# Kernel tuning notes

Hardware: AMD Instinct MI355X
Metric: run time of the kernel (lower is better)

The kernel has to match this reference:

```python
import jax, jax.numpy as jnp
import numpy as np

B, S, D, H = 4, 2048, 1024, 16
DK = D // H
THETA = 10000.0


def _rope(x, token_positions):
    # x: [b, h, s, d_k]; token_positions: [s] int
    half = x.shape[-1] // 2
    freqs = 1.0 / (THETA ** (2.0 * jnp.arange(half, dtype=jnp.float32) / x.shape[-1]))
    angles = token_positions.astype(jnp.float32)[:, None] * freqs[None, :]  # [s, half]
    cos, sin = jnp.cos(angles), jnp.sin(angles)
    x1 = x[..., 0::2]  # interleaved pairing: (d/2, 2)
    x2 = x[..., 1::2]
    r1 = x1 * cos - x2 * sin
    r2 = x2 * cos + x1 * sin
    return jnp.stack([r1, r2], axis=-1).reshape(x.shape)


def setup_inputs() -> dict:
    key = jax.random.key(0)
    ks = jax.random.split(key, 5)
    std_io = np.sqrt(2.0 / (D + D)).astype(np.float32)
    return {
        "x": jax.random.normal(ks[0], (B, S, D), dtype=jnp.float32),
        "token_positions": jnp.arange(S, dtype=jnp.int32),
        "Wq": jax.random.normal(ks[1], (D, D), dtype=jnp.float32) * std_io,
        "Wk": jax.random.normal(ks[2], (D, D), dtype=jnp.float32) * std_io,
        "Wv": jax.random.normal(ks[3], (D, D), dtype=jnp.float32) * std_io,
        "Wo": jax.random.normal(ks[4], (D, D), dtype=jnp.float32) * std_io,
    }


def reference(x, token_positions, Wq, Wk, Wv, Wo):
    b, s, d = x.shape
    # Linear uses W: [out, in] -> y = x @ W.T
    def proj(W):
        y = jnp.einsum('bsd,od->bso', x, W)
        return y.reshape(b, s, H, DK).transpose(0, 2, 1, 3)  # [b,h,s,dk]
    q, k, v = proj(Wq), proj(Wk), proj(Wv)
    q = _rope(q, token_positions)
    k = _rope(k, token_positions)
    scores = jnp.einsum('bhqd,bhkd->bhqk', q, k) / jnp.sqrt(jnp.float32(DK))
    causal = jnp.tril(jnp.ones((s, s), dtype=bool))
    scores = jnp.where(causal, scores, -jnp.inf)
    attn = jax.nn.softmax(scores, axis=-1)
    out = jnp.einsum('bhqk,bhkd->bhqd', attn, v)
    out = out.transpose(0, 2, 1, 3).reshape(b, s, d)
    return jnp.einsum('bsd,od->bso', out, Wo)
```

## Files before the change

### kernel.cpp

```cpp
#include <hip/hip_runtime.h>
#include <math.h>

#define B_ 4
#define S_ 2048
#define D_ 1024
#define H_ 16
#define DK_ 64
#define SCALE_ 0.125f
#define THETA_ 10000.0f
#define LOG2E_ 1.44269504f

typedef unsigned short ushort_t;
typedef __attribute__((ext_vector_type(8))) short bf16x8;
typedef __attribute__((ext_vector_type(4))) float f32x4;

__device__ __forceinline__ ushort_t f2bf(float f) {
    union { float f; unsigned u; } v; v.f = f;
    unsigned r = (v.u + 0x7FFFu + ((v.u >> 16) & 1u)) >> 16;
    return (ushort_t)r;
}

#define GLOAD_LDS16(gptr, lptr)                                                   \
    __builtin_amdgcn_global_load_lds(                                             \
        (const __attribute__((address_space(1))) unsigned int*)(gptr),            \
        (__attribute__((address_space(3))) unsigned int*)(lptr), 16, 0, 0)

__global__ __launch_bounds__(256) void cast_f32_bf16(const float* __restrict__ in,
                                                     ushort_t* __restrict__ out, int n) {
    int i = (blockIdx.x * 256 + threadIdx.x) * 4;
    if (i >= n) return;
    float4 v = *reinterpret_cast<const float4*>(in + i);
    unsigned lo = (unsigned)f2bf(v.x) | ((unsigned)f2bf(v.y) << 16);
    unsigned hi = (unsigned)f2bf(v.z) | ((unsigned)f2bf(v.w) << 16);
    uint2 u; u.x = lo; u.y = hi;
    *reinterpret_cast<uint2*>(out + i) = u;
}

__global__ __launch_bounds__(256) void build_rope(const int* __restrict__ pos,
                                                  float2* __restrict__ tab) {
    int i = blockIdx.x * 256 + threadIdx.x;
    int s = i >> 5, p = i & 31;
    float freq = powf(THETA_, -2.0f * (float)p / 64.0f);
    float a = (float)pos[s] * freq;
    tab[i] = make_float2(cosf(a), sinf(a));
}

template <int MODE>
__global__ __launch_bounds__(256) void gemm_bf16(const ushort_t* __restrict__ A,
                                                 const ushort_t* __restrict__ W,
                                                 const float2* __restrict__ tab,
                                                 float qscale,
                                                 float* __restrict__ outF,
                                                 ushort_t* __restrict__ outB) {
    __shared__ ushort_t Asl[128 * 32];
    __shared__ ushort_t Bsl[128 * 32];

    const int t = threadIdx.x;
    const int lane = t & 63;
    const int w = t >> 6;
    const int lr = lane & 15;
    const int lg = lane >> 4;

    const int bid = blockIdx.x;
    const int swz = (bid & 7) * 64 + (bid >> 3);
    const int m0 = (swz >> 3) * 128;
    const int n0 = (swz & 7) * 128;

    const int wr = w >> 1;
    const int wc = w & 1;

    f32x4 acc[4][4] = {};

    for (int k0 = 0; k0 < D_; k0 += 32) {
#pragma unroll
        for (int i = 0; i < 2; ++i) {
            const int off = w * 2048 + i * 1024 + lane * 16;
            const int row = off >> 6;
            const int col = (off & 63) >> 1;
            GLOAD_LDS16(A + (size_t)(m0 + row) * D_ + k0 + col, Asl + (w * 1024 + i * 512));
            GLOAD_LDS16(W + (size_t)(n0 + row) * D_ + k0 + col, Bsl + (w * 1024 + i * 512));
        }
        __syncthreads();

        bf16x8 af[4], bfr[4];
#pragma unroll
        for (int x = 0; x < 4; ++x) {
            af[x]  = *reinterpret_cast<const bf16x8*>(&Asl[(wr * 64 + x * 16 + lr) * 32 + lg * 8]);
            bfr[x] = *reinterpret_cast<const bf16x8*>(&Bsl[(wc * 64 + x * 16 + lr) * 32 + lg * 8]);
        }
#pragma unroll
        for (int mi = 0; mi < 4; ++mi)
#pragma unroll
            for (int ni = 0; ni < 4; ++ni)
                acc[mi][ni] = __builtin_amdgcn_mfma_f32_16x16x32_bf16(af[mi], bfr[ni], acc[mi][ni], 0, 0, 0);
        __syncthreads();
    }

#pragma unroll
    for (int mi = 0; mi < 4; ++mi) {
#pragma unroll
        for (int r = 0; r < 4; ++r) {
            const int m = m0 + wr * 64 + mi * 16 + lg * 4 + r;
            const int bb = m >> 11;
            const int s = m & (S_ - 1);
#pragma unroll
            for (int ni = 0; ni < 4; ++ni) {
                const int n = n0 + wc * 64 + ni * 16 + lr;
                float v = acc[mi][ni][r];
                if (MODE == 0) {
                    outF[(size_t)m * D_ + n] = v;
                } else {
                    const int h = n >> 6, dk = n & 63;
                    if (MODE == 2) {
                        v *= qscale;
                        const float2 cs = tab[s * 32 + (dk >> 1)];
                        const float part = __shfl_xor(v, 1, 64);
                        v = (dk & 1) ? fmaf(v, cs.x, part * cs.y)
                                     : fmaf(v, cs.x, -part * cs.y);
                    }
                    outB[(((size_t)bb * H_ + h) * S_ + s) * DK_ + dk] = f2bf(v);
                }
            }
        }
    }
}

__global__ __launch_bounds__(256) void attn_mfma(const ushort_t* __restrict__ Q,
                                                 const ushort_t* __restrict__ K,
                                                 const ushort_t* __restrict__ V,
                                                 ushort_t* __restrict__ O) {
    __shared__ ushort_t Ks[2][64 * 64];
    __shared__ ushort_t Vt[64 * 64];
    __shared__ ushort_t Pl[128 * 64];

    const int t = threadIdx.x;
    const int lane = t & 63;
    const int w = t >> 6;
    const int lr = lane & 15;
    const int lg = lane >> 4;

    const int bid = blockIdx.x;
    const int swz = (bid & 7) * 64 + (bid >> 3);
    const int bh = swz >> 3;
    const int p  = swz & 7;

    const ushort_t* Kbase = K + (size_t)bh * S_ * DK_;
    const ushort_t* Vbase = V + (size_t)bh * S_ * DK_;
    const int bb = bh >> 4, h = bh & 15;

    const int dk8 = (t & 7) * 8;
    const int kv2 = (t >> 3) * 2;

    bf16x8 ones;
#pragma unroll
    for (int j = 0; j < 8; ++j) ones[j] = (short)0x3F80;

    bf16x8 vpre0, vpre1;

    for (int ph = 0; ph < 2; ++ph) {
        const int qt = ph ? (15 - p) : p;
        const int q0 = qt * 128;
        const int nt = 2 * qt + 2;

        const ushort_t* Qbase = Q + ((size_t)bh * S_ + q0 + w * 32) * DK_;
        bf16x8 qf[2][2];
#pragma unroll
        for (int rf = 0; rf < 2; ++rf)
#pragma unroll
            for (int kf = 0; kf < 2; ++kf)
                qf[rf][kf] = *reinterpret_cast<const bf16x8*>(
                    Qbase + (size_t)(rf * 16 + lr) * DK_ + kf * 32 + lg * 8);

        f32x4 acc[2][4] = {};
        f32x4 accl[2] = {};
        float mrow[2] = {-INFINITY, -INFINITY};

#pragma unroll
        for (int it = 0; it < 2; ++it) {
            const int slotbase = w * 64 + it * 256;
            const int slot = slotbase + lane;
            const int row = slot >> 3;
            const int c16 = (slot & 7) ^ (row & 7);
            GLOAD_LDS16(Kbase + (size_t)row * DK_ + c16 * 8, &Ks[0][slotbase * 8]);
        }
        {
            const ushort_t* Vsrc = Vbase + (size_t)kv2 * DK_ + dk8;
            vpre0 = *reinterpret_cast<const bf16x8*>(Vsrc);
            vpre1 = *reinterpret_cast<const bf16x8*>(Vsrc + DK_);
        }
        __syncthreads();

        int cur = 0;
        for (int kt = 0; kt < nt; ++kt) {
#pragma unroll
            for (int j = 0; j < 8; ++j) {
                const int row = dk8 + j;
                unsigned pk = (unsigned)(ushort_t)vpre0[j] | ((unsigned)(ushort_t)vpre1[j] << 16);
                *reinterpret_cast<unsigned*>((char*)Vt + row * 128 + ((kv2 * 2) ^ (j << 4))) = pk;
            }
            __syncthreads();

            if (kt + 1 < nt) {
                const ushort_t* Ksrc = Kbase + (size_t)(kt + 1) * 64 * DK_;
#pragma unroll
                for (int it = 0; it < 2; ++it) {
                    const int slotbase = w * 64 + it * 256;
                    const int slot = slotbase + lane;
                    const int row = slot >> 3;
                    const int c16 = (slot & 7) ^ (row & 7);
                    GLOAD_LDS16(Ksrc + (size_t)row * DK_ + c16 * 8, &Ks[cur ^ 1][slotbase * 8]);
                }
                const ushort_t* Vsrc = Vbase + (size_t)((kt + 1) * 64 + kv2) * DK_ + dk8;
                vpre0 = *reinterpret_cast<const bf16x8*>(Vsrc);
                vpre1 = *reinterpret_cast<const bf16x8*>(Vsrc + DK_);
            }

            bf16x8 kb[4][2];
#pragma unroll
            for (int nf = 0; nf < 4; ++nf)
#pragma unroll
                for (int kf = 0; kf < 2; ++kf)
                    kb[nf][kf] = *reinterpret_cast<const bf16x8*>(
                        (char*)Ks[cur] + (nf * 16 + lr) * 128 + (((kf * 4 + lg) ^ (lr & 7)) << 4));

            f32x4 sT[2][4];
#pragma unroll
            for (int rf = 0; rf < 2; ++rf)
#pragma unroll
                for (int nf = 0; nf < 4; ++nf) {
                    f32x4 z = {};
                    z = __builtin_amdgcn_mfma_f32_16x16x32_bf16(kb[nf][0], qf[rf][0], z, 0, 0, 0);
                    z = __builtin_amdgcn_mfma_f32_16x16x32_bf16(kb[nf][1], qf[rf][1], z, 0, 0, 0);
                    sT[rf][nf] = z;
                }

            if (kt >= nt - 2) {
#pragma unroll
                for (int rf = 0; rf < 2; ++rf) {
                    const int q = q0 + w * 32 + rf * 16 + lr;
#pragma unroll
                    for (int nf = 0; nf < 4; ++nf)
#pragma unroll
                        for (int r = 0; r < 4; ++r) {
                            const int kv = kt * 64 + nf * 16 + lg * 4 + r;
                            if (kv > q) sT[rf][nf][r] = -INFINITY;
                        }
                }
            }

#pragma unroll
            for (int rf = 0; rf < 2; ++rf) {
                float m4 = -INFINITY;
#pragma unroll
                for (int nf = 0; nf < 4; ++nf)
#pragma unroll
                    for (int r = 0; r < 4; ++r) m4 = fmaxf(m4, sT[rf][nf][r]);
                m4 = fmaxf(m4, __shfl_xor(m4, 16, 64));
                m4 = fmaxf(m4, __shfl_xor(m4, 32, 64));
                const float mn = fmaxf(mrow[rf], m4);
                if (mn > mrow[rf]) {
                    const float corr = __builtin_amdgcn_exp2f(mrow[rf] - mn);
                    mrow[rf] = mn;
#pragma unroll
                    for (int r = 0; r < 4; ++r) accl[rf][r] *= corr;
#pragma unroll
                    for (int df = 0; df < 4; ++df)
#pragma unroll
                        for (int r = 0; r < 4; ++r) acc[rf][df][r] *= corr;
                }
            }

#pragma unroll
            for (int rf = 0; rf < 2; ++rf) {
                const int prow = w * 32 + rf * 16 + lr;
                char* prowp = (char*)Pl + prow * 128;
#pragma unroll
                for (int nf = 0; nf < 4; ++nf) {
                    const float p0 = __builtin_amdgcn_exp2f(sT[rf][nf][0] - mrow[rf]);
                    const float p1 = __builtin_amdgcn_exp2f(sT[rf][nf][1] - mrow[rf]);
                    const float p2 = __builtin_amdgcn_exp2f(sT[rf][nf][2] - mrow[rf]);
                    const float p3 = __builtin_amdgcn_exp2f(sT[rf][nf][3] - mrow[rf]);
                    uint2 pk;
                    pk.x = (unsigned)f2bf(p0) | ((unsigned)f2bf(p1) << 16);
                    pk.y = (unsigned)f2bf(p2) | ((unsigned)f2bf(p3) << 16);
                    const int chunk = (nf * 2 + (lg >> 1)) ^ (lr & 7);
                    *reinterpret_cast<uint2*>(prowp + (chunk << 4) + (lg & 1) * 8) = pk;
                }
            }

            bf16x8 pfr[2][2];
#pragma unroll
            for (int rf = 0; rf < 2; ++rf) {
                const int prow = w * 32 + rf * 16 + lr;
#pragma unroll
                for (int kf = 0; kf < 2; ++kf)
                    pfr[rf][kf] = *reinterpret_cast<const bf16x8*>(
                        (char*)Pl + prow * 128 + (((kf * 4 + lg) ^ (lr & 7)) << 4));
            }
            bf16x8 vtf[4][2];
#pragma unroll
            for (int df = 0; df < 4; ++df)
#pragma unroll
                for (int kf = 0; kf < 2; ++kf)
                    vtf[df][kf] = *reinterpret_cast<const bf16x8*>(
                        (char*)Vt + (df * 16 + lr) * 128 + (((kf * 4 + lg) ^ (lr & 7)) << 4));

#pragma unroll
            for (int rf = 0; rf < 2; ++rf) {
#pragma unroll
                for (int kf = 0; kf < 2; ++kf)
                    accl[rf] = __builtin_amdgcn_mfma_f32_16x16x32_bf16(ones, pfr[rf][kf], accl[rf], 0, 0, 0);
#pragma unroll
                for (int df = 0; df < 4; ++df)
#pragma unroll
                    for (int kf = 0; kf < 2; ++kf)
                        acc[rf][df] = __builtin_amdgcn_mfma_f32_16x16x32_bf16(vtf[df][kf], pfr[rf][kf], acc[rf][df], 0, 0, 0);
            }

            __syncthreads();
            cur ^= 1;
        }

#pragma unroll
        for (int rf = 0; rf < 2; ++rf) {
            const float inv = 1.0f / accl[rf][0];
            const int q = q0 + w * 32 + rf * 16 + lr;
            ushort_t* Orow = O + ((size_t)bb * S_ + q) * D_ + h * DK_;
#pragma unroll
            for (int df = 0; df < 4; ++df) {
                unsigned lo = (unsigned)f2bf(acc[rf][df][0] * inv) | ((unsigned)f2bf(acc[rf][df][1] * inv) << 16);
                unsigned hi = (unsigned)f2bf(acc[rf][df][2] * inv) | ((unsigned)f2bf(acc[rf][df][3] * inv) << 16);
                *reinterpret_cast<unsigned*>(Orow + df * 16 + lg * 4)     = lo;
                *reinterpret_cast<unsigned*>(Orow + df * 16 + lg * 4 + 2) = hi;
            }
        }
    }
}

extern "C" void kernel_launch(void* const* d_in, const int* in_sizes, int n_in,
                              void* d_out, int out_size, void* d_ws, size_t ws_size,
                              hipStream_t stream) {
    const float* x  = (const float*)d_in[0];
    const int*   tp = (const int*)d_in[1];
    const float* Wq = (const float*)d_in[2];
    const float* Wk = (const float*)d_in[3];
    const float* Wv = (const float*)d_in[4];
    const float* Wo = (const float*)d_in[5];
    float* out = (float*)d_out;

    char* ws = (char*)d_ws;
    ushort_t* Xb  = (ushort_t*)(ws);
    ushort_t* Wqb = (ushort_t*)(ws + (16ull << 20));
    ushort_t* Wkb = (ushort_t*)(ws + (18ull << 20));
    ushort_t* Wvb = (ushort_t*)(ws + (20ull << 20));
    ushort_t* Wob = (ushort_t*)(ws + (22ull << 20));
    ushort_t* Qb  = (ushort_t*)(ws + (24ull << 20));
    ushort_t* Kb  = (ushort_t*)(ws + (40ull << 20));
    ushort_t* Vb  = (ushort_t*)(ws + (56ull << 20));
    ushort_t* Ao  = (ushort_t*)(ws + (72ull << 20));
    float2*   tab = (float2*)(ws + (88ull << 20));

    const int NX = B_ * S_ * D_;
    const int NW = D_ * D_;
    cast_f32_bf16<<<NX / 1024, 256, 0, stream>>>(x, Xb, NX);
    cast_f32_bf16<<<NW / 1024, 256, 0, stream>>>(Wq, Wqb, NW);
    cast_f32_bf16<<<NW / 1024, 256, 0, stream>>>(Wk, Wkb, NW);
    cast_f32_bf16<<<NW / 1024, 256, 0, stream>>>(Wv, Wvb, NW);
    cast_f32_bf16<<<NW / 1024, 256, 0, stream>>>(Wo, Wob, NW);
    build_rope<<<(S_ * 32) / 256, 256, 0, stream>>>(tp, tab);

    gemm_bf16<2><<<512, 256, 0, stream>>>(Xb, Wqb, tab, SCALE_ * LOG2E_, nullptr, Qb);
    gemm_bf16<2><<<512, 256, 0, stream>>>(Xb, Wkb, tab, 1.0f, nullptr, Kb);
    gemm_bf16<1><<<512, 256, 0, stream>>>(Xb, Wvb, tab, 1.0f, nullptr, Vb);

    attn_mfma<<<512, 256, 0, stream>>>(Qb, Kb, Vb, Ao);

    gemm_bf16<0><<<512, 256, 0, stream>>>(Ao, Wob, tab, 1.0f, out, nullptr);
}
```

Before: 219.8 us.

## Lazy softmax rescale with threshold, perm-based bf16 packing, new V swizzle

```diff
diff --git a/kernel.cpp b/kernel.cpp
--- a/kernel.cpp
+++ b/kernel.cpp
@@ -9,6 +9,7 @@
 #define SCALE_ 0.125f
 #define THETA_ 10000.0f
 #define LOG2E_ 1.44269504f
+#define THR_ 8.0f
 
 typedef unsigned short ushort_t;
 typedef __attribute__((ext_vector_type(8))) short bf16x8;
@@ -19,6 +20,12 @@
     unsigned r = (v.u + 0x7FFFu + ((v.u >> 16) & 1u)) >> 16;
     return (ushort_t)r;
 }
+
+__device__ __forceinline__ unsigned permpk(float lo, float hi) {
+    return __builtin_amdgcn_perm(__float_as_uint(hi), __float_as_uint(lo), 0x07060302u);
+}
+
+__device__ __forceinline__ int vswz(int row) { return (row & 7) ^ ((row >> 3) & 3); }
 
 #define GLOAD_LDS16(gptr, lptr)                                                   \
     __builtin_amdgcn_global_load_lds(                                             \
@@ -125,10 +132,10 @@
     }
 }
 
-__global__ __launch_bounds__(256) void attn_mfma(const ushort_t* __restrict__ Q,
-                                                 const ushort_t* __restrict__ K,
-                                                 const ushort_t* __restrict__ V,
-                                                 ushort_t* __restrict__ O) {
+__global__ __launch_bounds__(256, 4) void attn_mfma(const ushort_t* __restrict__ Q,
+                                                    const ushort_t* __restrict__ K,
+                                                    const ushort_t* __restrict__ V,
+                                                    ushort_t* __restrict__ O) {
     __shared__ ushort_t Ks[2][64 * 64];
     __shared__ ushort_t Vt[64 * 64];
     __shared__ ushort_t Pl[128 * 64];
@@ -192,11 +199,17 @@
 
         int cur = 0;
         for (int kt = 0; kt < nt; ++kt) {
-#pragma unroll
-            for (int j = 0; j < 8; ++j) {
-                const int row = dk8 + j;
-                unsigned pk = (unsigned)(ushort_t)vpre0[j] | ((unsigned)(ushort_t)vpre1[j] << 16);
-                *reinterpret_cast<unsigned*>((char*)Vt + row * 128 + ((kv2 * 2) ^ (j << 4))) = pk;
+            {
+                const unsigned* aw = reinterpret_cast<const unsigned*>(&vpre0);
+                const unsigned* bw = reinterpret_cast<const unsigned*>(&vpre1);
+#pragma unroll
+                for (int j = 0; j < 8; ++j) {
+                    const int row = dk8 + j;
+                    const unsigned sel = (j & 1) ? 0x07060302u : 0x05040100u;
+                    const unsigned pk = __builtin_amdgcn_perm(bw[j >> 1], aw[j >> 1], sel);
+                    *reinterpret_cast<unsigned*>(
+                        (char*)Vt + row * 128 + ((kv2 * 2) ^ (vswz(row) << 4))) = pk;
+                }
             }
             __syncthreads();
 
@@ -257,10 +270,9 @@
                     for (int r = 0; r < 4; ++r) m4 = fmaxf(m4, sT[rf][nf][r]);
                 m4 = fmaxf(m4, __shfl_xor(m4, 16, 64));
                 m4 = fmaxf(m4, __shfl_xor(m4, 32, 64));
-                const float mn = fmaxf(mrow[rf], m4);
-                if (mn > mrow[rf]) {
-                    const float corr = __builtin_amdgcn_exp2f(mrow[rf] - mn);
-                    mrow[rf] = mn;
+                if (m4 > mrow[rf] + THR_) {
+                    const float corr = __builtin_amdgcn_exp2f(mrow[rf] - m4);
+                    mrow[rf] = m4;
 #pragma unroll
                     for (int r = 0; r < 4; ++r) accl[rf][r] *= corr;
 #pragma unroll
@@ -281,8 +293,8 @@
                     const float p2 = __builtin_amdgcn_exp2f(sT[rf][nf][2] - mrow[rf]);
                     const float p3 = __builtin_amdgcn_exp2f(sT[rf][nf][3] - mrow[rf]);
                     uint2 pk;
-                    pk.x = (unsigned)f2bf(p0) | ((unsigned)f2bf(p1) << 16);
-                    pk.y = (unsigned)f2bf(p2) | ((unsigned)f2bf(p3) << 16);
+                    pk.x = permpk(p0, p1);
+                    pk.y = permpk(p2, p3);
                     const int chunk = (nf * 2 + (lg >> 1)) ^ (lr & 7);
                     *reinterpret_cast<uint2*>(prowp + (chunk << 4) + (lg & 1) * 8) = pk;
                 }
@@ -303,7 +315,7 @@
 #pragma unroll
                 for (int kf = 0; kf < 2; ++kf)
                     vtf[df][kf] = *reinterpret_cast<const bf16x8*>(
-                        (char*)Vt + (df * 16 + lr) * 128 + (((kf * 4 + lg) ^ (lr & 7)) << 4));
+                        (char*)Vt + (df * 16 + lr) * 128 + (((kf * 4 + lg) ^ vswz(df * 16 + lr)) << 4));
 
 #pragma unroll
             for (int rf = 0; rf < 2; ++rf) {
```

Result: slower. 248.8 us (+13.2%).
